# Optimization experiments

Measured on AMD Instinct MI355X. Metric: run time of the kernel, lower is better.

The kernel has to match this reference:

```python
import jax, jax.numpy as jnp
import numpy as np

N_EMBD = 768
N_HEAD = 12
HEAD_DIM = N_EMBD // N_HEAD
HIDDEN = 4 * N_EMBD
B, T = 4, 2048
EPS = 1e-5


def setup_inputs() -> dict:
    key = jax.random.key(0)
    ks = jax.random.split(key, 7)
    s = lambda fan_in: 1.0 / np.sqrt(fan_in)
    return {
        "x": jax.random.normal(ks[0], (B, T, N_EMBD), dtype=jnp.float32),
        "ln1_g": jnp.ones((N_EMBD,), jnp.float32),
        "ln1_b": jnp.zeros((N_EMBD,), jnp.float32),
        "W_attn": jax.random.normal(ks[1], (N_EMBD, 3 * N_EMBD), jnp.float32) * s(N_EMBD),
        "W_o": jax.random.normal(ks[2], (N_EMBD, N_EMBD), jnp.float32) * s(N_EMBD),
        "ln2_g": jnp.ones((N_EMBD,), jnp.float32),
        "ln2_b": jnp.zeros((N_EMBD,), jnp.float32),
        "W_fc": jax.random.normal(ks[3], (N_EMBD, HIDDEN), jnp.float32) * s(N_EMBD),
        "W_proj": jax.random.normal(ks[4], (HIDDEN, N_EMBD), jnp.float32) * s(HIDDEN),
    }


def _layernorm(x, g, b):
    mu = jnp.mean(x, axis=-1, keepdims=True)
    var = jnp.mean(jnp.square(x - mu), axis=-1, keepdims=True)
    return (x - mu) * jax.lax.rsqrt(var + EPS) * g + b


def _attention(x, W_attn, W_o):
    b, t, c = x.shape
    qkv = x @ W_attn  # [B,T,3C]
    q, k, v = jnp.split(qkv, 3, axis=-1)
    # [B,H,T,D]
    q = q.reshape(b, t, N_HEAD, HEAD_DIM).transpose(0, 2, 1, 3)
    k = k.reshape(b, t, N_HEAD, HEAD_DIM).transpose(0, 2, 1, 3)
    v = v.reshape(b, t, N_HEAD, HEAD_DIM).transpose(0, 2, 1, 3)
    scale = 1.0 / jnp.sqrt(jnp.float32(HEAD_DIM))
    att = jnp.einsum("bhqd,bhkd->bhqk", q, k) * scale  # [B,H,T,T]
    causal = jnp.arange(t)[:, None] >= jnp.arange(t)[None, :]
    att = jnp.where(causal, att, -jnp.inf)
    att = jax.nn.softmax(att, axis=-1)
    y = jnp.einsum("bhqk,bhkd->bhqd", att, v)
    y = y.transpose(0, 2, 1, 3).reshape(b, t, c)
    return y @ W_o


def reference(x, ln1_g, ln1_b, W_attn, W_o, ln2_g, ln2_b, W_fc, W_proj):
    x = x + _attention(_layernorm(x, ln1_g, ln1_b), W_attn, W_o)
    h = _layernorm(x, ln2_g, ln2_b)
    h = jax.nn.gelu(h @ W_fc, approximate=False) @ W_proj  # torch nn.GELU() is exact erf gelu
    return x + h
```

## Files before the change

kernel.cpp:

```cpp
#include <hip/hip_runtime.h>
#include <cstdint>
#include <cstddef>

#define B_ 4
#define T_ 2048
#define C_ 768
#define H_ 12
#define D_ 64
#define M_ (B_*T_)
#define C3_ 2304
#define HID_ 3072

typedef unsigned short ushort_t;
typedef __bf16 bf16x8_t __attribute__((ext_vector_type(8)));
typedef float f32x4 __attribute__((ext_vector_type(4)));

typedef const __attribute__((address_space(1))) void* gas_ptr;
typedef __attribute__((address_space(3))) void* las_ptr;

__device__ __forceinline__ void gload_lds16(const ushort_t* g, ushort_t* l) {
  __builtin_amdgcn_global_load_lds((gas_ptr)g, (las_ptr)l, 16, 0, 0);
}

__device__ __forceinline__ float bf2f(ushort_t h) {
  union { unsigned int u; float f; } cv; cv.u = ((unsigned int)h) << 16; return cv.f;
}
__device__ __forceinline__ ushort_t f2bf(float f) {
  union { float f; unsigned int u; } cv; cv.f = f;
  unsigned int u = cv.u;
  unsigned int r = (u + 0x7FFFu + ((u >> 16) & 1u)) >> 16;
  return (ushort_t)r;
}
__device__ __forceinline__ ushort_t f2bf_trunc(float f) {
  union { float f; unsigned int u; } cv; cv.f = f;
  return (ushort_t)(cv.u >> 16);
}

__global__ __launch_bounds__(256) void transpose_k(const float* __restrict__ in,
                                                   ushort_t* __restrict__ out, int K, int N) {
  __shared__ ushort_t tile[32][33];
  int nx = threadIdx.x, ky = threadIdx.y;
  int n0 = blockIdx.x * 32, k0 = blockIdx.y * 32;
#pragma unroll
  for (int i = 0; i < 4; i++)
    tile[ky + i * 8][nx] = f2bf(in[(size_t)(k0 + ky + i * 8) * N + n0 + nx]);
  __syncthreads();
#pragma unroll
  for (int i = 0; i < 4; i++)
    out[(size_t)(n0 + ky + i * 8) * K + k0 + nx] = tile[nx][ky + i * 8];
}

__global__ __launch_bounds__(256) void vtrans_k(const ushort_t* __restrict__ qkv,
                                                ushort_t* __restrict__ vg) {
  __shared__ ushort_t tile[32][33];
  int nx = threadIdx.x, ky = threadIdx.y;
  int t0 = blockIdx.x * 32, d0 = blockIdx.y * 32;
  int bh = blockIdx.z;
  int b = bh / H_, h = bh % H_;
  const ushort_t* src = qkv + (size_t)b * T_ * C3_ + 2 * C_ + h * D_;
#pragma unroll
  for (int i = 0; i < 4; i++)
    tile[ky + i * 8][nx] = src[(size_t)(t0 + ky + i * 8) * C3_ + d0 + nx];
  __syncthreads();
  ushort_t* dst = vg + (size_t)bh * D_ * T_;
#pragma unroll
  for (int i = 0; i < 4; i++)
    dst[(size_t)(d0 + ky + i * 8) * T_ + t0 + nx] = tile[nx][ky + i * 8];
}

__global__ __launch_bounds__(256) void ln_k(const float* __restrict__ x, const float* __restrict__ g,
                                            const float* __restrict__ bb, ushort_t* __restrict__ out) {
  __shared__ float red[8];
  int row = blockIdx.x, t = threadIdx.x;
  const float* xr = x + (size_t)row * C_;
  float v0 = xr[t], v1 = xr[t + 256], v2 = xr[t + 512];
  float s = v0 + v1 + v2;
  float s2 = v0 * v0 + v1 * v1 + v2 * v2;
#pragma unroll
  for (int m = 32; m >= 1; m >>= 1) { s += __shfl_xor(s, m); s2 += __shfl_xor(s2, m); }
  int w = t >> 6;
  if ((t & 63) == 0) { red[w * 2] = s; red[w * 2 + 1] = s2; }
  __syncthreads();
  s = red[0] + red[2] + red[4] + red[6];
  s2 = red[1] + red[3] + red[5] + red[7];
  float mu = s * (1.f / C_);
  float var = s2 * (1.f / C_) - mu * mu;
  float rstd = rsqrtf(var + 1e-5f);
  out[(size_t)row * C_ + t]       = f2bf((v0 - mu) * rstd * g[t] + bb[t]);
  out[(size_t)row * C_ + t + 256] = f2bf((v1 - mu) * rstd * g[t + 256] + bb[t + 256]);
  out[(size_t)row * C_ + t + 512] = f2bf((v2 - mu) * rstd * g[t + 512] + bb[t + 512]);
}

#define MFMA16(d, a, b) d = __builtin_amdgcn_mfma_f32_16x16x32_bf16(a, b, d, 0, 0, 0)

template <int EPI>
__global__ void gemm_bt_k(const ushort_t* __restrict__ A,
                          const ushort_t* __restrict__ Bt,
                          const float* __restrict__ res,
                          void* __restrict__ outp,
                          int N, int K) {
  __shared__ __align__(16) ushort_t As[3][128][32];
  __shared__ __align__(16) ushort_t Bs[3][128][32];
  int t = threadIdx.x;

  int nwg = (int)(gridDim.x * gridDim.y);
  int orig = (int)(blockIdx.y * gridDim.x + blockIdx.x);
  int swz = (nwg & 7) ? orig : ((orig & 7) * (nwg >> 3) + (orig >> 3));
  int bx = swz % (int)gridDim.x, by = swz / (int)gridDim.x;
  int bn = bx * 128, bm = by * 128;

  int lane = t & 63, w = t >> 6;
  int wm = (w >> 1) * 64, wn = (w & 1) * 64;
  int lm = lane & 15;

  int lr = lane >> 2;
  int lc = (((lane & 3) ^ ((lane >> 3) & 3)) * 8);
  int cx = (((lane >> 4) ^ ((lane >> 1) & 3)) * 8);

  const ushort_t* ga0 = A  + (size_t)(bm + w * 16 + lr) * K + lc;
  const ushort_t* gb0 = Bt + (size_t)(bn + w * 16 + lr) * K + lc;
  const size_t kstep64 = (size_t)64 * K;

  const f32x4 fz = {0.f, 0.f, 0.f, 0.f};
  f32x4 acc00 = fz, acc01 = fz, acc02 = fz, acc03 = fz;
  f32x4 acc10 = fz, acc11 = fz, acc12 = fz, acc13 = fz;
  f32x4 acc20 = fz, acc21 = fz, acc22 = fz, acc23 = fz;
  f32x4 acc30 = fz, acc31 = fz, acc32 = fz, acc33 = fz;

#define STAGE(BUF, TILE) do {                                   \
    int ko_ = (TILE) * 32;                                      \
    gload_lds16(ga0 + ko_, &As[BUF][w * 16][0]);                \
    gload_lds16(ga0 + kstep64 + ko_, &As[BUF][w * 16 + 64][0]); \
    gload_lds16(gb0 + ko_, &Bs[BUF][w * 16][0]);                \
    gload_lds16(gb0 + kstep64 + ko_, &Bs[BUF][w * 16 + 64][0]); \
  } while (0)

#define COMPUTE(BUF) do {                                            \
    bf16x8_t af0 = *(const bf16x8_t*)&As[BUF][wm + lm][cx];          \
    bf16x8_t af1 = *(const bf16x8_t*)&As[BUF][wm + 16 + lm][cx];     \
    bf16x8_t af2 = *(const bf16x8_t*)&As[BUF][wm + 32 + lm][cx];     \
    bf16x8_t af3 = *(const bf16x8_t*)&As[BUF][wm + 48 + lm][cx];     \
    bf16x8_t bg0 = *(const bf16x8_t*)&Bs[BUF][wn + lm][cx];          \
    bf16x8_t bg1 = *(const bf16x8_t*)&Bs[BUF][wn + 16 + lm][cx];     \
    bf16x8_t bg2 = *(const bf16x8_t*)&Bs[BUF][wn + 32 + lm][cx];     \
    bf16x8_t bg3 = *(const bf16x8_t*)&Bs[BUF][wn + 48 + lm][cx];     \
    MFMA16(acc00, af0, bg0); MFMA16(acc01, af0, bg1); MFMA16(acc02, af0, bg2); MFMA16(acc03, af0, bg3); \
    MFMA16(acc10, af1, bg0); MFMA16(acc11, af1, bg1); MFMA16(acc12, af1, bg2); MFMA16(acc13, af1, bg3); \
    MFMA16(acc20, af2, bg0); MFMA16(acc21, af2, bg1); MFMA16(acc22, af2, bg2); MFMA16(acc23, af2, bg3); \
    MFMA16(acc30, af3, bg0); MFMA16(acc31, af3, bg1); MFMA16(acc32, af3, bg2); MFMA16(acc33, af3, bg3); \
  } while (0)

  int nsteps = K >> 5;
  STAGE(0, 0);
  STAGE(1, 1);
  for (int s = 0; s < nsteps; s += 3) {
    STAGE(2, s + 2);
    asm volatile("s_waitcnt vmcnt(8)" ::: "memory");
    __builtin_amdgcn_s_barrier();
    asm volatile("" ::: "memory");
    COMPUTE(0);
    asm volatile("" ::: "memory");
    __builtin_amdgcn_s_barrier();
    if (s + 3 < nsteps) {
      STAGE(0, s + 3);
      asm volatile("s_waitcnt vmcnt(8)" ::: "memory");
    } else {
      asm volatile("s_waitcnt vmcnt(4)" ::: "memory");
    }
    __builtin_amdgcn_s_barrier();
    asm volatile("" ::: "memory");
    COMPUTE(1);
    asm volatile("" ::: "memory");
    __builtin_amdgcn_s_barrier();
    if (s + 4 < nsteps) {
      STAGE(1, s + 4);
      asm volatile("s_waitcnt vmcnt(8)" ::: "memory");
    } else {
      asm volatile("s_waitcnt vmcnt(0)" ::: "memory");
    }
    __builtin_amdgcn_s_barrier();
    asm volatile("" ::: "memory");
    COMPUTE(2);
    asm volatile("" ::: "memory");
    __builtin_amdgcn_s_barrier();
  }
#undef STAGE
#undef COMPUTE

  int rowb = bm + wm + (lane >> 4) * 4;
  int colb = bn + wn + lm;

#define ST(vv, row, jj) do { \
    float v = (vv); \
    size_t idx = (size_t)(row) * N + colb + (jj) * 16; \
    if constexpr (EPI == 0) { ((ushort_t*)outp)[idx] = f2bf(v); } \
    else if constexpr (EPI == 1) { ((float*)outp)[idx] = v + res[idx]; } \
    else { float gl = 0.5f * v * (1.0f + erff(v * 0.70710678118654752f)); \
           ((ushort_t*)outp)[idx] = f2bf(gl); } \
  } while (0)
#define STROW(a0, a1, a2, a3, row, rr) \
    ST(a0[rr], row, 0); ST(a1[rr], row, 1); ST(a2[rr], row, 2); ST(a3[rr], row, 3);
#define STBLK(a0, a1, a2, a3, rbase) \
    STROW(a0, a1, a2, a3, (rbase), 0) STROW(a0, a1, a2, a3, (rbase) + 1, 1) \
    STROW(a0, a1, a2, a3, (rbase) + 2, 2) STROW(a0, a1, a2, a3, (rbase) + 3, 3)

  STBLK(acc00, acc01, acc02, acc03, rowb)
  STBLK(acc10, acc11, acc12, acc13, rowb + 16)
  STBLK(acc20, acc21, acc22, acc23, rowb + 32)
  STBLK(acc30, acc31, acc32, acc33, rowb + 48)
#undef ST
#undef STROW
#undef STBLK
}

__device__ __forceinline__ void stage64(const ushort_t* __restrict__ g, size_t strideE,
                                        ushort_t* l, int w, int lane) {
  int rl = lane >> 3;
  int ce = ((lane & 7) ^ rl) << 3;
  const ushort_t* g0 = g + (size_t)(w * 16 + rl) * strideE + ce;
  gload_lds16(g0, l + (size_t)(w * 16) * 64);
  const ushort_t* g1 = g + (size_t)(w * 16 + 8 + rl) * strideE + ce;
  gload_lds16(g1, l + (size_t)(w * 16 + 8) * 64);
}

__global__ __launch_bounds__(256, 3) void attn_k(const ushort_t* __restrict__ qkv,
                                                 const ushort_t* __restrict__ vg,
                                                 ushort_t* __restrict__ y) {
  __shared__ __align__(16) ushort_t Ks[2][64][64];
  __shared__ __align__(16) ushort_t Vs[2][64][64];
  __shared__ __align__(16) ushort_t Ps[4][16][72];

  int t = threadIdx.x;
  int w = t >> 6, lane = t & 63;
  int lm = lane & 15, qq = lane >> 4, q8 = qq * 8;
  int bh = blockIdx.x;
  int qt = (int)gridDim.y - 1 - (int)blockIdx.y;
  int b = bh / H_, h = bh % H_;

  size_t baserow = (size_t)b * T_;
  const ushort_t* qkvb = qkv + baserow * C3_ + h * D_;
  const ushort_t* kbase = qkvb + C_;
  const ushort_t* vbase = vg + (size_t)bh * D_ * T_;

  int qrow0 = qt * 64 + w * 16;
  const ushort_t* qp = qkvb + (size_t)(qrow0 + lm) * C3_ + q8;
  bf16x8_t aq0 = *(const bf16x8_t*)(qp);
  bf16x8_t aq1 = *(const bf16x8_t*)(qp + 32);
  __builtin_amdgcn_s_waitcnt(0);

  const f32x4 fz = {0.f, 0.f, 0.f, 0.f};
  f32x4 aO0 = fz, aO1 = fz, aO2 = fz, aO3 = fz;
  f32x4 lsum = fz;

  const float SC = 0.125f * 1.44269504088896340736f;

#define BODY(CUR, KT, MASKED)                                                   \
  {                                                                             \
    const char* Kb = (const char*)&Ks[CUR][0][0];                               \
    const char* Vb = (const char*)&Vs[CUR][0][0];                               \
    const int rsw = (lm & 7) << 4;                                              \
    const int c0 = (qq * 16) ^ rsw;                                             \
    const int c1 = (64 + qq * 16) ^ rsw;                                        \
    bf16x8_t kf[8], vv[8];                                                      \
    _Pragma("unroll") for (int j = 0; j < 4; j++) {                             \
      int rb = (j * 16 + lm) << 7;                                              \
      kf[2*j]   = *(const bf16x8_t*)(Kb + rb + c0);                             \
      kf[2*j+1] = *(const bf16x8_t*)(Kb + rb + c1);                             \
      vv[2*j]   = *(const bf16x8_t*)(Vb + rb + c0);                             \
      vv[2*j+1] = *(const bf16x8_t*)(Vb + rb + c1);                             \
    }                                                                           \
    f32x4 sa0 = fz, sa1 = fz, sa2 = fz, sa3 = fz;                               \
    MFMA16(sa0, aq0, kf[0]); MFMA16(sa0, aq1, kf[1]);                           \
    MFMA16(sa1, aq0, kf[2]); MFMA16(sa1, aq1, kf[3]);                           \
    MFMA16(sa2, aq0, kf[4]); MFMA16(sa2, aq1, kf[5]);                           \
    MFMA16(sa3, aq0, kf[6]); MFMA16(sa3, aq1, kf[7]);                           \
    _Pragma("unroll") for (int j = 0; j < 4; j++) {                             \
      f32x4 sj = (j == 0) ? sa0 : (j == 1) ? sa1 : (j == 2) ? sa2 : sa3;        \
      _Pragma("unroll") for (int r2 = 0; r2 < 4; r2++) {                        \
        float v = sj[r2] * SC;                                                  \
        if (MASKED && (j * 16 + lm) > (w * 16 + qq * 4 + r2)) v = -1e30f;       \
        float p = exp2f(v);                                                     \
        lsum[r2] += p;                                                          \
        Ps[w][qq * 4 + r2][j * 16 + lm] = f2bf_trunc(p);                        \
      }                                                                         \
    }                                                                           \
    {                                                                           \
      bf16x8_t ap_lo = *(const bf16x8_t*)&Ps[w][lm][q8];                        \
      bf16x8_t ap_hi = *(const bf16x8_t*)&Ps[w][lm][32 + q8];                   \
      MFMA16(aO0, ap_lo, vv[0]); MFMA16(aO0, ap_hi, vv[1]);                     \
      MFMA16(aO1, ap_lo, vv[2]); MFMA16(aO1, ap_hi, vv[3]);                     \
      MFMA16(aO2, ap_lo, vv[4]); MFMA16(aO2, ap_hi, vv[5]);                     \
      MFMA16(aO3, ap_lo, vv[6]); MFMA16(aO3, ap_hi, vv[7]);                     \
    }                                                                           \
  }

  stage64(kbase, C3_, &Ks[0][0][0], w, lane);
  stage64(vbase, T_, &Vs[0][0][0], w, lane);
  int cur = 0;
  for (int kt = 0; kt <= qt; ++kt) {
    if (kt < qt) {
      stage64(kbase + (size_t)(kt + 1) * 64 * C3_, C3_, &Ks[cur ^ 1][0][0], w, lane);
      stage64(vbase + (size_t)(kt + 1) * 64,       T_,  &Vs[cur ^ 1][0][0], w, lane);
      asm volatile("s_waitcnt vmcnt(4)" ::: "memory");
    } else {
      asm volatile("s_waitcnt vmcnt(0)" ::: "memory");
    }
    __builtin_amdgcn_s_barrier();
    asm volatile("" ::: "memory");
    if (kt == qt) { BODY(cur, kt, true) }
    else          { BODY(cur, kt, false) }
    asm volatile("" ::: "memory");
    __builtin_amdgcn_s_barrier();
    cur ^= 1;
  }
#undef BODY

#pragma unroll
  for (int r2 = 0; r2 < 4; r2++) {
    float s = lsum[r2];
    s += __shfl_xor(s, 1);
    s += __shfl_xor(s, 2);
    s += __shfl_xor(s, 4);
    s += __shfl_xor(s, 8);
    float inv = 1.f / s;
    size_t orow = (baserow + qrow0 + qq * 4 + r2) * C_ + h * D_;
    y[orow + lm]      = f2bf(aO0[r2] * inv);
    y[orow + 16 + lm] = f2bf(aO1[r2] * inv);
    y[orow + 32 + lm] = f2bf(aO2[r2] * inv);
    y[orow + 48 + lm] = f2bf(aO3[r2] * inv);
  }
}

extern "C" void kernel_launch(void* const* d_in, const int* in_sizes, int n_in,
                              void* d_out, int out_size, void* d_ws, size_t ws_size,
                              hipStream_t stream) {
  (void)in_sizes; (void)n_in; (void)out_size; (void)ws_size;
  const float* x      = (const float*)d_in[0];
  const float* ln1_g  = (const float*)d_in[1];
  const float* ln1_b  = (const float*)d_in[2];
  const float* W_attn = (const float*)d_in[3];
  const float* W_o    = (const float*)d_in[4];
  const float* ln2_g  = (const float*)d_in[5];
  const float* ln2_b  = (const float*)d_in[6];
  const float* W_fc   = (const float*)d_in[7];
  const float* W_proj = (const float*)d_in[8];

  char* ws = (char*)d_ws;
  ushort_t* big  = (ushort_t*)(ws);
  ushort_t* Vg   = (ushort_t*)(ws + 37748736);
  ushort_t* tmp  = (ushort_t*)(ws + 50331648);
  float*    x2   = (float*)   (ws + 62914560);
  ushort_t* Wat  = (ushort_t*)(ws + 88080384);
  ushort_t* Wot  = (ushort_t*)(ws + 91619328);
  ushort_t* Wfct = (ushort_t*)(ws + 92798976);
  ushort_t* Wpt  = (ushort_t*)(ws + 97517568);

  dim3 tb(32, 8);
  transpose_k<<<dim3(C3_ / 32, C_ / 32), tb, 0, stream>>>(W_attn, Wat, C_, C3_);
  transpose_k<<<dim3(C_ / 32, C_ / 32), tb, 0, stream>>>(W_o, Wot, C_, C_);
  transpose_k<<<dim3(HID_ / 32, C_ / 32), tb, 0, stream>>>(W_fc, Wfct, C_, HID_);
  transpose_k<<<dim3(C_ / 32, HID_ / 32), tb, 0, stream>>>(W_proj, Wpt, HID_, C_);

  ln_k<<<M_, 256, 0, stream>>>(x, ln1_g, ln1_b, tmp);
  gemm_bt_k<0><<<dim3(C3_ / 128, M_ / 128), 256, 0, stream>>>(tmp, Wat, nullptr, big, C3_, C_);
  vtrans_k<<<dim3(T_ / 32, D_ / 32, B_ * H_), tb, 0, stream>>>(big, Vg);
  attn_k<<<dim3(B_ * H_, T_ / 64), 256, 0, stream>>>(big, Vg, tmp);
  gemm_bt_k<1><<<dim3(C_ / 128, M_ / 128), 256, 0, stream>>>(tmp, Wot, x, x2, C_, C_);
  ln_k<<<M_, 256, 0, stream>>>(x2, ln2_g, ln2_b, tmp);
  gemm_bt_k<2><<<dim3(HID_ / 128, M_ / 128), 256, 0, stream>>>(tmp, Wfct, nullptr, big, HID_, C_);
  gemm_bt_k<1><<<dim3(C_ / 128, M_ / 128), 256, 0, stream>>>(big, Wpt, x2, d_out, C_, HID_);
}
```

Baseline: 379.9 us.

## Deepen GEMM LDS pipeline to four stages and use a polynomial erf GELU

The bf16 GEMM now keeps four LDS stages instead of three. The next tile's loads are issued right after a single barrier per k-step, so there is one barrier per step rather than two and global-to-LDS copies overlap the MFMA work. The GELU epilogue replaces the library erff with an Abramowitz-Stegun polynomial using a hardware reciprocal and exp2, which makes the fc-layer epilogue cheaper. In exchange, LDS use per block grows to 64KB, which may lower occupancy, and the erf approximation adds a small error of about 1e-7.

```diff
diff --git a/kernel.cpp b/kernel.cpp
--- a/kernel.cpp
+++ b/kernel.cpp
@@ -34,6 +34,17 @@
 __device__ __forceinline__ ushort_t f2bf_trunc(float f) {
   union { float f; unsigned int u; } cv; cv.f = f;
   return (ushort_t)(cv.u >> 16);
+}
+
+__device__ __forceinline__ float gelu_f(float v) {
+  float z = fabsf(v) * 0.70710678118654752f;
+  float t = __builtin_amdgcn_rcpf(fmaf(0.3275911f, z, 1.0f));
+  float e = exp2f(z * z * -1.44269504088896340736f);
+  float p = t * fmaf(t, fmaf(t, fmaf(t, fmaf(t, 1.061405429f, -1.453152027f),
+                                     1.421413741f), -0.284496736f), 0.254829592f);
+  float ea = fmaf(-p, e, 1.0f);
+  float er = copysignf(ea, v);
+  return 0.5f * v * (1.0f + er);
 }
 
 __global__ __launch_bounds__(256) void transpose_k(const float* __restrict__ in,
@@ -99,8 +110,8 @@
                           const float* __restrict__ res,
                           void* __restrict__ outp,
                           int N, int K) {
-  __shared__ __align__(16) ushort_t As[3][128][32];
-  __shared__ __align__(16) ushort_t Bs[3][128][32];
+  __shared__ __align__(16) ushort_t As[4][128][32];
+  __shared__ __align__(16) ushort_t Bs[4][128][32];
   int t = threadIdx.x;
 
   int nwg = (int)(gridDim.x * gridDim.y);
@@ -150,40 +161,41 @@
     MFMA16(acc30, af3, bg0); MFMA16(acc31, af3, bg1); MFMA16(acc32, af3, bg2); MFMA16(acc33, af3, bg3); \
   } while (0)
 
+#define FENCE asm volatile("" ::: "memory")
+
   int nsteps = K >> 5;
   STAGE(0, 0);
   STAGE(1, 1);
-  for (int s = 0; s < nsteps; s += 3) {
-    STAGE(2, s + 2);
+  STAGE(2, 2);
+  for (int s = 0; s < nsteps; s += 4) {
     asm volatile("s_waitcnt vmcnt(8)" ::: "memory");
     __builtin_amdgcn_s_barrier();
-    asm volatile("" ::: "memory");
+    FENCE;
+    STAGE(3, s + 3);
     COMPUTE(0);
-    asm volatile("" ::: "memory");
-    __builtin_amdgcn_s_barrier();
-    if (s + 3 < nsteps) {
-      STAGE(0, s + 3);
-      asm volatile("s_waitcnt vmcnt(8)" ::: "memory");
-    } else {
-      asm volatile("s_waitcnt vmcnt(4)" ::: "memory");
-    }
-    __builtin_amdgcn_s_barrier();
-    asm volatile("" ::: "memory");
+    FENCE;
+    asm volatile("s_waitcnt vmcnt(8)" ::: "memory");
+    __builtin_amdgcn_s_barrier();
+    FENCE;
+    if (s + 4 < nsteps) STAGE(0, s + 4);
     COMPUTE(1);
-    asm volatile("" ::: "memory");
-    __builtin_amdgcn_s_barrier();
-    if (s + 4 < nsteps) {
-      STAGE(1, s + 4);
-      asm volatile("s_waitcnt vmcnt(8)" ::: "memory");
-    } else {
-      asm volatile("s_waitcnt vmcnt(0)" ::: "memory");
-    }
-    __builtin_amdgcn_s_barrier();
-    asm volatile("" ::: "memory");
+    FENCE;
+    if (s + 4 < nsteps) { asm volatile("s_waitcnt vmcnt(8)" ::: "memory"); }
+    else                { asm volatile("s_waitcnt vmcnt(4)" ::: "memory"); }
+    __builtin_amdgcn_s_barrier();
+    FENCE;
+    if (s + 5 < nsteps) STAGE(1, s + 5);
     COMPUTE(2);
-    asm volatile("" ::: "memory");
-    __builtin_amdgcn_s_barrier();
+    FENCE;
+    if (s + 4 < nsteps) { asm volatile("s_waitcnt vmcnt(8)" ::: "memory"); }
+    else                { asm volatile("s_waitcnt vmcnt(0)" ::: "memory"); }
+    __builtin_amdgcn_s_barrier();
+    FENCE;
+    if (s + 6 < nsteps) STAGE(2, s + 6);
+    COMPUTE(3);
+    FENCE;
   }
+#undef FENCE
 #undef STAGE
 #undef COMPUTE
 
@@ -195,8 +207,7 @@
     size_t idx = (size_t)(row) * N + colb + (jj) * 16; \
     if constexpr (EPI == 0) { ((ushort_t*)outp)[idx] = f2bf(v); } \
     else if constexpr (EPI == 1) { ((float*)outp)[idx] = v + res[idx]; } \
-    else { float gl = 0.5f * v * (1.0f + erff(v * 0.70710678118654752f)); \
-           ((ushort_t*)outp)[idx] = f2bf(gl); } \
+    else { ((ushort_t*)outp)[idx] = f2bf(gelu_f(v)); } \
   } while (0)
 #define STROW(a0, a1, a2, a3, row, rr) \
     ST(a0[rr], row, 0); ST(a1[rr], row, 1); ST(a2[rr], row, 2); ST(a3[rr], row, 3);
```

Result: slower. 396.6 us (+4.4%).
